# Optimization experiments

Measured on AMD Instinct MI355X. Metric: run time of the kernel, lower is better.

Reference implementation:

```python
import jax, jax.numpy as jnp
import numpy as np

B, T, I, H, L = 128, 512, 512, 1024, 2
KEEP = 0.9  # 1 - dropout_rate


def setup_inputs() -> dict:
    key = jax.random.key(0)
    ks = jax.random.split(key, 13)
    s = 0.02
    bern = lambda k, shape: (jax.random.bernoulli(k, KEEP, shape) / KEEP).astype(jnp.float32)
    return {
        "x": jax.random.normal(ks[0], (B, T, I), dtype=jnp.float32),
        "W_ih0": jax.random.normal(ks[1], (4 * H, I), dtype=jnp.float32) * s,
        "W_hh0": jax.random.normal(ks[2], (4 * H, H), dtype=jnp.float32) * s,
        "b_ih0": jax.random.normal(ks[3], (4 * H,), dtype=jnp.float32) * s,
        "b_hh0": jax.random.normal(ks[4], (4 * H,), dtype=jnp.float32) * s,
        "W_ih1": jax.random.normal(ks[5], (4 * H, H), dtype=jnp.float32) * s,
        "W_hh1": jax.random.normal(ks[6], (4 * H, H), dtype=jnp.float32) * s,
        "b_ih1": jax.random.normal(ks[7], (4 * H,), dtype=jnp.float32) * s,
        "b_hh1": jax.random.normal(ks[8], (4 * H,), dtype=jnp.float32) * s,
        "out_mask": bern(ks[9], (L, B, H)),
        "h_mask": bern(ks[10], (L, B, H)),
        "c_mask": bern(ks[11], (L, B, H)),
    }


def _run_layer(x_tbi, W_ih, W_hh, b_ih, b_hh, om, hm, cm):
    """x_tbi: [T,B,in]; masks: [B,H]. Returns ([T,B,H] outputs, final (h,c))."""
    h0 = jnp.zeros((x_tbi.shape[1], H), dtype=x_tbi.dtype)
    c0 = jnp.zeros_like(h0)
    # precompute input projections for all timesteps: [T,B,4H]
    xg = jnp.einsum('tbi,gi->tbg', x_tbi, W_ih) + b_ih + b_hh

    def step(carry, xg_t):
        h, c = carry
        gates = xg_t + h @ W_hh.T  # [B,4H]
        i, f, g, o = jnp.split(gates, 4, axis=-1)
        i, f, o = jax.nn.sigmoid(i), jax.nn.sigmoid(f), jax.nn.sigmoid(o)
        g = jnp.tanh(g)
        c2 = f * c + i * g
        h2 = o * jnp.tanh(c2)
        out = h2 * om
        return (h2 * hm, c2 * cm), out

    (hf, cf), ys = jax.lax.scan(step, (h0, c0), xg)
    return ys, (hf, cf)


def reference(x, W_ih0, W_hh0, b_ih0, b_hh0, W_ih1, W_hh1, b_ih1, b_hh1,
              out_mask, h_mask, c_mask):
    layers = [(W_ih0, W_hh0, b_ih0, b_hh0), (W_ih1, W_hh1, b_ih1, b_hh1)]
    xt = jnp.transpose(x, (1, 0, 2))  # [T,B,I]
    for l, (Wi, Wh, bi, bh) in enumerate(layers):
        xt, (hf, cf) = _run_layer(xt, Wi, Wh, bi, bh,
                                  out_mask[l], h_mask[l], c_mask[l])
    out = jnp.transpose(xt, (1, 0, 2))  # [B,T,H]
    return out, (hf[None], cf[None])
```

## Files before the change

### kernel.cpp

```cpp
#include <hip/hip_runtime.h>

#define B_  128
#define T_  512
#define I_  512
#define H_  1024
#define G4  4096
#define SLOT 262144L
#define SENTW 0xFFFFFFFFu

typedef __attribute__((ext_vector_type(8))) short   short8;
typedef __attribute__((ext_vector_type(4))) short   short4v;
typedef __attribute__((ext_vector_type(4))) float   f32x4;
typedef unsigned long long u64;

__device__ __forceinline__ float bf2f(short u){
  return __uint_as_float(((unsigned)(unsigned short)u) << 16);
}
__device__ __forceinline__ short f2bf(float f){
  unsigned u = __float_as_uint(f);
  unsigned r = (u + 0x7FFFu + ((u >> 16) & 1u)) >> 16;
  return (short)r;
}
__device__ __forceinline__ float sigm(float x){ return 1.0f/(1.0f + __expf(-x)); }
__device__ __forceinline__ float tanh_(float x){ return 1.0f - 2.0f/(__expf(2.0f*x) + 1.0f); }
__device__ __forceinline__ bool okq(u64 a){
  return ((unsigned)a != SENTW) & ((unsigned)(a >> 32) != SENTW);
}

__global__ __launch_bounds__(256) void cvt_bf16(const float* __restrict__ in,
                                                short* __restrict__ out, int nq){
  int i = blockIdx.x*256 + threadIdx.x;
  if (i >= nq) return;
  float4 v = ((const float4*)in)[i];
  short4v o; o.x = f2bf(v.x); o.y = f2bf(v.y); o.z = f2bf(v.z); o.w = f2bf(v.w);
  ((short4v*)out)[i] = o;
}

__global__ __launch_bounds__(256) void swz_whh(const float* __restrict__ W,
                                               short* __restrict__ out){
  int c = blockIdx.x*256 + threadIdx.x;
  int l = c & 63, ks = (c >> 6) & 15, ct = (c >> 10) & 1, wvv = (c >> 11) & 7, jb = c >> 14;
  int g = wvv >> 1, kh = wvv & 1;
  long row = (long)(g*1024 + jb*32 + ct*16 + (l & 15));
  int col = kh*512 + ks*32 + (l >> 4)*8;
  const float* src = W + row*H_ + col;
  short8 o;
#pragma unroll
  for (int e = 0; e < 8; ++e) o[e] = f2bf(src[e]);
  ((short8*)out)[c] = o;
}

template<int K>
__global__ __launch_bounds__(256) void proj_gemm(const short* __restrict__ A,
                                                 const short* __restrict__ W,
                                                 const float* __restrict__ bih,
                                                 const float* __restrict__ bhh,
                                                 short* __restrict__ C){
  __shared__ __align__(16) short lds[2][2][128*40];
  const int tid = threadIdx.x;
  const int l  = tid & 63, wv = tid >> 6;
  const int wm = wv >> 1,  wn = wv & 1;
  const int nt = blockIdx.x, mt = blockIdx.y;
  const int r0 = tid >> 2, cb = (tid & 3) * 8;
  const short* Ab = A + (long)(mt*128 + r0)*K + cb;
  const short* Wb = W + (long)(nt*128 + r0)*K + cb;
  const int lo  = r0*40 + cb;
  const int lo2 = lo + 64*40;
  const int NK = K/32;

  short8 pa0 = *(const short8*)(Ab);
  short8 pa1 = *(const short8*)(Ab + 64*K);
  short8 pb0 = *(const short8*)(Wb);
  short8 pb1 = *(const short8*)(Wb + 64*K);
  *(short8*)&lds[0][0][lo]  = pa0;
  *(short8*)&lds[0][0][lo2] = pa1;
  *(short8*)&lds[0][1][lo]  = pb0;
  *(short8*)&lds[0][1][lo2] = pb1;

  f32x4 acc[4][4];
  f32x4 z = {0.f,0.f,0.f,0.f};
#pragma unroll
  for (int i = 0; i < 4; ++i)
#pragma unroll
    for (int j = 0; j < 4; ++j) acc[i][j] = z;

  for (int kt = 0; kt < NK; ++kt){
    __syncthreads();
    if (kt + 1 < NK){
      pa0 = *(const short8*)(Ab + (kt+1)*32);
      pa1 = *(const short8*)(Ab + (kt+1)*32 + 64*K);
      pb0 = *(const short8*)(Wb + (kt+1)*32);
      pb1 = *(const short8*)(Wb + (kt+1)*32 + 64*K);
    }
    const short* As = lds[kt & 1][0];
    const short* Bs = lds[kt & 1][1];
    short8 bfr[4];
#pragma unroll
    for (int nf = 0; nf < 4; ++nf)
      bfr[nf] = *(const short8*)&Bs[(wn*64 + nf*16 + (l & 15))*40 + (l >> 4)*8];
#pragma unroll
    for (int mf = 0; mf < 4; ++mf){
      short8 af = *(const short8*)&As[(wm*64 + mf*16 + (l & 15))*40 + (l >> 4)*8];
#pragma unroll
      for (int nf = 0; nf < 4; ++nf)
        acc[mf][nf] = __builtin_amdgcn_mfma_f32_16x16x32_bf16(af, bfr[nf], acc[mf][nf], 0, 0, 0);
    }
    if (kt + 1 < NK){
      int nb = (kt + 1) & 1;
      *(short8*)&lds[nb][0][lo]  = pa0;
      *(short8*)&lds[nb][0][lo2] = pa1;
      *(short8*)&lds[nb][1][lo]  = pb0;
      *(short8*)&lds[nb][1][lo2] = pb1;
    }
  }

  __syncthreads();
  short* cst = (short*)&lds[0][0][0];
#pragma unroll
  for (int nf = 0; nf < 4; ++nf){
    int nc = wn*64 + nf*16 + (l & 15);
    int n  = nt*128 + nc;
    float bs = bih[n] + bhh[n];
#pragma unroll
    for (int mf = 0; mf < 4; ++mf){
#pragma unroll
      for (int r = 0; r < 4; ++r){
        int mr = wm*64 + mf*16 + (l >> 4)*4 + r;
        cst[mr*132 + nc] = f2bf(acc[mf][nf][r] + bs);
      }
    }
  }
  __syncthreads();
  const long m0 = (long)mt*128;
  const int  n0 = nt*128;
#pragma unroll
  for (int i = 0; i < 8; ++i){
    int sid = i*256 + tid;
    int mr = sid >> 4, seg = sid & 15;
    *(short8*)&C[(m0 + mr)*G4 + n0 + seg*8] = *(const short8*)&cst[mr*132 + seg*8];
  }
}

template<int LAYER, bool RING>
__global__ __launch_bounds__(512, 2) void lstm_scan(
    short* __restrict__ hring,
    const short* __restrict__ Wsw, const short* __restrict__ xg,
    const float* __restrict__ om, const float* __restrict__ hm, const float* __restrict__ cm,
    short* __restrict__ out0, float* __restrict__ dout,
    int* __restrict__ flags)
{
  const int tid = threadIdx.x;
  const int l = tid & 63, wv = tid >> 6;
  const int bt = blockIdx.x, jb = blockIdx.y;

  short8 w0[16], w1[16];
  {
    const short8* wp = (const short8*)Wsw + ((long)((jb*8 + wv)*2)*16)*64 + l;
#pragma unroll
    for (int ks = 0; ks < 16; ++ks) w0[ks] = wp[ks*64];
#pragma unroll
    for (int ks = 0; ks < 16; ++ks) w1[ks] = wp[(16 + ks)*64];
    f32x4* wf0 = (f32x4*)w0;
    f32x4* wf1 = (f32x4*)w1;
#pragma unroll
    for (int i = 0; i < 16; ++i){ asm volatile("" : "+v"(wf0[i])); asm volatile("" : "+v"(wf1[i])); }
  }

  const int idx = wv*8 + (l >> 3);
  const int bl  = idx & 15;
  const int jl  = ((idx >> 4) << 3) + (l & 7);
  const int jcol = jb*32 + jl;
  const long bj = (long)(bt*16 + bl)*H_ + jcol;
  const float mo = om[bj], mh = hm[bj], mc = cm[bj];
  float c = 0.f;
  const int ct_r = jl >> 4;
  const int lane_src = (jl & 15) + ((bl >> 2) << 4);
  const int rr = bl & 3;
  const int kh = wv & 1;

  __shared__ __align__(16) short hbuf[2048*8];
  __shared__ float red[16*264];
  __shared__ __align__(16) short sstage[512];
  int* flbase = flags + (long)bt*T_*32;

  const long go0 = (long)(wv*256 + 0*64 + l)*2;
  const long go1 = (long)(wv*256 + 1*64 + l)*2;
  const long go2 = (long)(wv*256 + 2*64 + l)*2;
  const long go3 = (long)(wv*256 + 3*64 + l)*2;

  const long xbase = (long)(bt*16 + bl)*T_*G4 + jcol;
  short xv0 = xg[xbase], xv1 = xg[xbase + H_], xv2 = xg[xbase + 2*H_], xv3 = xg[xbase + 3*H_];

  for (int t = 0; t < T_; ++t){
    const long slotoff  = RING ? (long)t*SLOT     : (long)(t & 1)*SLOT;
    const long nslotoff = RING ? (long)(t+1)*SLOT : (long)((t+1) & 1)*SLOT;

    if (t > 0){
      const u64* hp = (const u64*)((const char*)hring + slotoff + (long)bt*32768);
      if constexpr (RING){
        u64 q0=0,q1=0,q2=0,q3=0,q4=0,q5=0,q6=0,q7=0;
        int ok = 0, spins = 0;
        while (true){
          if (!(ok & 1)){
            u64 a = __hip_atomic_load(hp + go0,     __ATOMIC_RELAXED, __HIP_MEMORY_SCOPE_AGENT);
            u64 b = __hip_atomic_load(hp + go0 + 1, __ATOMIC_RELAXED, __HIP_MEMORY_SCOPE_AGENT);
            if (okq(a) & okq(b)){ q0 = a; q1 = b; ok |= 1; }
          }
          if (!(ok & 2)){
            u64 a = __hip_atomic_load(hp + go1,     __ATOMIC_RELAXED, __HIP_MEMORY_SCOPE_AGENT);
            u64 b = __hip_atomic_load(hp + go1 + 1, __ATOMIC_RELAXED, __HIP_MEMORY_SCOPE_AGENT);
            if (okq(a) & okq(b)){ q2 = a; q3 = b; ok |= 2; }
          }
          if (!(ok & 4)){
            u64 a = __hip_atomic_load(hp + go2,     __ATOMIC_RELAXED, __HIP_MEMORY_SCOPE_AGENT);
            u64 b = __hip_atomic_load(hp + go2 + 1, __ATOMIC_RELAXED, __HIP_MEMORY_SCOPE_AGENT);
            if (okq(a) & okq(b)){ q4 = a; q5 = b; ok |= 4; }
          }
          if (!(ok & 8)){
            u64 a = __hip_atomic_load(hp + go3,     __ATOMIC_RELAXED, __HIP_MEMORY_SCOPE_AGENT);
            u64 b = __hip_atomic_load(hp + go3 + 1, __ATOMIC_RELAXED, __HIP_MEMORY_SCOPE_AGENT);
            if (okq(a) & okq(b)){ q6 = a; q7 = b; ok |= 8; }
          }
          if (ok == 15) break;
          if (++spins > (1 << 20)) break;
          if (spins > 2) __builtin_amdgcn_s_sleep(2);
        }
        union { u64 u[2]; short8 s; } c0, c1, c2_, c3;
        c0.u[0] = q0; c0.u[1] = q1;  c1.u[0] = q2; c1.u[1] = q3;
        c2_.u[0] = q4; c2_.u[1] = q5; c3.u[0] = q6; c3.u[1] = q7;
        *(short8*)&hbuf[(wv*256 +   0 + l)*8] = c0.s;
        *(short8*)&hbuf[(wv*256 +  64 + l)*8] = c1.s;
        *(short8*)&hbuf[(wv*256 + 128 + l)*8] = c2_.s;
        *(short8*)&hbuf[(wv*256 + 192 + l)*8] = c3.s;
      } else {
        short8 vv[4];
#pragma unroll
        for (int i = 0; i < 4; ++i){
          const u64* ap = hp + (long)(wv*256 + i*64 + l)*2;
          union { u64 q[2]; short8 s; } uu;
          uu.q[0] = __hip_atomic_load(ap,     __ATOMIC_RELAXED, __HIP_MEMORY_SCOPE_AGENT);
          uu.q[1] = __hip_atomic_load(ap + 1, __ATOMIC_RELAXED, __HIP_MEMORY_SCOPE_AGENT);
          vv[i] = uu.s;
        }
#pragma unroll
        for (int i = 0; i < 4; ++i)
          *(short8*)&hbuf[(wv*256 + i*64 + l)*8] = vv[i];
      }
      __syncthreads();

      f32x4 a00 = {0.f,0.f,0.f,0.f}, a01 = {0.f,0.f,0.f,0.f};
      f32x4 a10 = {0.f,0.f,0.f,0.f}, a11 = {0.f,0.f,0.f,0.f};
#pragma unroll
      for (int ks = 0; ks < 16; ++ks){
        short8 av = *(const short8*)&hbuf[((kh*16 + ks)*64 + l)*8];
        if (ks & 1){
          a01 = __builtin_amdgcn_mfma_f32_16x16x32_bf16(av, w0[ks], a01, 0, 0, 0);
          a11 = __builtin_amdgcn_mfma_f32_16x16x32_bf16(av, w1[ks], a11, 0, 0, 0);
        } else {
          a00 = __builtin_amdgcn_mfma_f32_16x16x32_bf16(av, w0[ks], a00, 0, 0, 0);
          a10 = __builtin_amdgcn_mfma_f32_16x16x32_bf16(av, w1[ks], a10, 0, 0, 0);
        }
      }
      f32x4 s0, s1;
#pragma unroll
      for (int r = 0; r < 4; ++r){ s0[r] = a00[r] + a01[r]; s1[r] = a10[r] + a11[r]; }
      *(f32x4*)&red[(wv*2 + 0)*264 + l*4] = s0;
      *(f32x4*)&red[(wv*2 + 1)*264 + l*4] = s1;
      __syncthreads();
    }

    float gate[4];
    short xvv[4] = {xv0, xv1, xv2, xv3};
#pragma unroll
    for (int g = 0; g < 4; ++g){
      float rv = 0.f;
      if (t > 0){
        rv = red[((g*2 + 0)*2 + ct_r)*264 + lane_src*4 + rr]
           + red[((g*2 + 1)*2 + ct_r)*264 + lane_src*4 + rr];
      }
      gate[g] = rv + bf2f(xvv[g]);
    }
    float ii = sigm(gate[0]);
    float ff = sigm(gate[1]);
    float gg = tanh_(gate[2]);
    float oo = sigm(gate[3]);
    float c2 = ff*c + ii*gg;
    float h2 = oo*tanh_(c2);
    c = c2*mc;
    float hn = h2*mh;

    if (t == T_ - 1){
      if (LAYER == 0){
        out0[((long)(bt*16 + bl)*T_ + t)*H_ + jcol] = f2bf(h2*mo);
      } else {
        dout[((long)(bt*16 + bl)*T_ + t)*H_ + jcol] = h2*mo;
        dout[(long)B_*T_*H_ + bj] = hn;
        dout[(long)B_*T_*H_ + (long)B_*H_ + bj] = c;
      }
      break;
    }

    sstage[wv*64 + l] = f2bf(hn);
    asm volatile("s_waitcnt lgkmcnt(0)" ::: "memory");
    __builtin_amdgcn_sched_barrier(0);
    if (l < 8){
      short8 pk = *(const short8*)&sstage[wv*64 + l*8];
      char* hdst = (char*)hring + nslotoff
                 + ((long)bt*2048 + jb*64 + wv*8 + l)*16;
      if constexpr (RING){
        asm volatile("global_store_dwordx4 %0, %1, off sc1" :: "v"(hdst), "v"(pk) : "memory");
      } else {
        union { short8 s; u64 q[2]; } uu; uu.s = pk;
        u64* qp = (u64*)hdst;
        __hip_atomic_store(qp,     uu.q[0], __ATOMIC_RELAXED, __HIP_MEMORY_SCOPE_AGENT);
        __hip_atomic_store(qp + 1, uu.q[1], __ATOMIC_RELAXED, __HIP_MEMORY_SCOPE_AGENT);
      }
    }
    if constexpr (!RING){
      asm volatile("s_waitcnt vmcnt(0)" ::: "memory");
      __syncthreads();
      if (tid == 0)
        __hip_atomic_store(&flbase[(long)t*32 + jb], 1,
                           __ATOMIC_RELAXED, __HIP_MEMORY_SCOPE_AGENT);
    }

    if (LAYER == 0){
      out0[((long)(bt*16 + bl)*T_ + t)*H_ + jcol] = f2bf(h2*mo);
    } else {
      dout[((long)(bt*16 + bl)*T_ + t)*H_ + jcol] = h2*mo;
    }
    {
      const short* xp = xg + xbase + (long)(t + 1)*G4;
      xv0 = xp[0]; xv1 = xp[H_]; xv2 = xp[2*H_]; xv3 = xp[3*H_];
    }

    if constexpr (!RING){
      const u64* fp = (const u64*)&flbase[(long)t*32];
      int spins = 0;
      while (true){
        int ok = 1;
        if (l < 16){
          u64 v = __hip_atomic_load(fp + l, __ATOMIC_RELAXED, __HIP_MEMORY_SCOPE_AGENT);
          ok = ((unsigned)v != 0u) & ((unsigned)(v >> 32) != 0u);
        }
        if (__all(ok)) break;
        if (++spins > (1 << 20)) break;
        if (spins > 8) __builtin_amdgcn_s_sleep(1);
      }
      __builtin_amdgcn_sched_barrier(0);
      __builtin_amdgcn_fence(__ATOMIC_ACQUIRE, "workgroup");
    }
  }
}

extern "C" void kernel_launch(void* const* d_in, const int* in_sizes, int n_in,
                              void* d_out, int out_size, void* d_ws, size_t ws_size,
                              hipStream_t stream){
  const float* x    = (const float*)d_in[0];
  const float* Wih0 = (const float*)d_in[1];
  const float* Whh0 = (const float*)d_in[2];
  const float* bih0 = (const float*)d_in[3];
  const float* bhh0 = (const float*)d_in[4];
  const float* Wih1 = (const float*)d_in[5];
  const float* Whh1 = (const float*)d_in[6];
  const float* bih1 = (const float*)d_in[7];
  const float* bhh1 = (const float*)d_in[8];
  const float* omsk = (const float*)d_in[9];
  const float* hmsk = (const float*)d_in[10];
  const float* cmsk = (const float*)d_in[11];
  float* out = (float*)d_out;

  char* p = (char*)d_ws;
  auto alloc = [&](size_t bytes)->char*{
    char* r = p; p += (bytes + 255) & ~(size_t)255; return r;
  };
  short* xg      = (short*)alloc((size_t)65536*4096*2);
  short* out0_bf = (short*)alloc((size_t)67108864*2);
  short* x_bf    = (short*)out0_bf;
  short* wih0_bf = (short*)alloc((size_t)2097152*2);
  short* wih1_bf = (short*)alloc((size_t)4194304*2);
  short* whh0_sw = (short*)alloc((size_t)4194304*2);
  short* whh1_sw = (short*)alloc((size_t)4194304*2);
  int*   flags0  = (int*)alloc((size_t)8*512*32*4);
  int*   flags1  = (int*)alloc((size_t)8*512*32*4);
  size_t fixed = (size_t)(p - (char*)d_ws);
  bool ring = (fixed + (size_t)512*SLOT) <= ws_size;
  size_t ringbytes = ring ? (size_t)512*SLOT : (size_t)2*SLOT;
  short* hring = (short*)alloc(ringbytes);
  if ((size_t)(p - (char*)d_ws) > ws_size) return;

  hipMemsetAsync(flags0, 0, (size_t)8*512*32*4, stream);
  hipMemsetAsync(flags1, 0, (size_t)8*512*32*4, stream);
  hipMemsetAsync(hring, 0xFF, ringbytes, stream);

  cvt_bf16<<<33554432/4/256, 256, 0, stream>>>(x,    x_bf,    33554432/4);
  cvt_bf16<<<2097152/4/256,  256, 0, stream>>>(Wih0, wih0_bf, 2097152/4);
  cvt_bf16<<<4194304/4/256,  256, 0, stream>>>(Wih1, wih1_bf, 4194304/4);
  swz_whh <<<524288/256,     256, 0, stream>>>(Whh0, whh0_sw);
  swz_whh <<<524288/256,     256, 0, stream>>>(Whh1, whh1_sw);

  proj_gemm<512><<<dim3(32, 512), 256, 0, stream>>>(x_bf, wih0_bf, bih0, bhh0, xg);
  if (ring)
    lstm_scan<0, true ><<<dim3(8, 32), 512, 0, stream>>>(hring, whh0_sw, xg,
        omsk, hmsk, cmsk, out0_bf, nullptr, flags0);
  else
    lstm_scan<0, false><<<dim3(8, 32), 512, 0, stream>>>(hring, whh0_sw, xg,
        omsk, hmsk, cmsk, out0_bf, nullptr, flags0);

  hipMemsetAsync(hring, 0xFF, ringbytes, stream);

  proj_gemm<1024><<<dim3(32, 512), 256, 0, stream>>>(out0_bf, wih1_bf, bih1, bhh1, xg);
  if (ring)
    lstm_scan<1, true ><<<dim3(8, 32), 512, 0, stream>>>(hring, whh1_sw, xg,
        omsk + 131072, hmsk + 131072, cmsk + 131072, nullptr, out, flags1);
  else
    lstm_scan<1, false><<<dim3(8, 32), 512, 0, stream>>>(hring, whh1_sw, xg,
        omsk + 131072, hmsk + 131072, cmsk + 131072, nullptr, out, flags1);
}
```

Before: 4.101 ms.

## Replace sentinel polling on LSTM ring data with per-wave ready marks

The ring path of the LSTM scan used to poll the hidden-state data itself until no 0xFF sentinel words remained. Now each wave writes a ready mark after storing its slice, and one wave per block polls the 256 marks before a barrier and plain loads of the hidden state. This removes the two large 0xFF memsets of the ring buffer and the per-element sentinel checks. In exchange it adds a block barrier and a second memory round trip per step, and correctness depends on the partial vmcnt wait ordering the h store before the mark store.

```diff
diff --git a/kernel.cpp b/kernel.cpp
--- a/kernel.cpp
+++ b/kernel.cpp
@@ -6,7 +6,6 @@
 #define H_  1024
 #define G4  4096
 #define SLOT 262144L
-#define SENTW 0xFFFFFFFFu
 
 typedef __attribute__((ext_vector_type(8))) short   short8;
 typedef __attribute__((ext_vector_type(4))) short   short4v;
@@ -23,9 +22,6 @@
 }
 __device__ __forceinline__ float sigm(float x){ return 1.0f/(1.0f + __expf(-x)); }
 __device__ __forceinline__ float tanh_(float x){ return 1.0f - 2.0f/(__expf(2.0f*x) + 1.0f); }
-__device__ __forceinline__ bool okq(u64 a){
-  return ((unsigned)a != SENTW) & ((unsigned)(a >> 32) != SENTW);
-}
 
 __global__ __launch_bounds__(256) void cvt_bf16(const float* __restrict__ in,
                                                 short* __restrict__ out, int nq){
@@ -147,6 +143,7 @@
     const short* __restrict__ Wsw, const short* __restrict__ xg,
     const float* __restrict__ om, const float* __restrict__ hm, const float* __restrict__ cm,
     short* __restrict__ out0, float* __restrict__ dout,
+    int* __restrict__ marks,
     int* __restrict__ flags)
 {
   const int tid = threadIdx.x;
@@ -183,11 +180,6 @@
   __shared__ __align__(16) short sstage[512];
   int* flbase = flags + (long)bt*T_*32;
 
-  const long go0 = (long)(wv*256 + 0*64 + l)*2;
-  const long go1 = (long)(wv*256 + 1*64 + l)*2;
-  const long go2 = (long)(wv*256 + 2*64 + l)*2;
-  const long go3 = (long)(wv*256 + 3*64 + l)*2;
-
   const long xbase = (long)(bt*16 + bl)*T_*G4 + jcol;
   short xv0 = xg[xbase], xv1 = xg[xbase + H_], xv2 = xg[xbase + 2*H_], xv3 = xg[xbase + 3*H_];
 
@@ -196,43 +188,31 @@
     const long nslotoff = RING ? (long)(t+1)*SLOT : (long)((t+1) & 1)*SLOT;
 
     if (t > 0){
-      const u64* hp = (const u64*)((const char*)hring + slotoff + (long)bt*32768);
       if constexpr (RING){
-        u64 q0=0,q1=0,q2=0,q3=0,q4=0,q5=0,q6=0,q7=0;
-        int ok = 0, spins = 0;
-        while (true){
-          if (!(ok & 1)){
-            u64 a = __hip_atomic_load(hp + go0,     __ATOMIC_RELAXED, __HIP_MEMORY_SCOPE_AGENT);
-            u64 b = __hip_atomic_load(hp + go0 + 1, __ATOMIC_RELAXED, __HIP_MEMORY_SCOPE_AGENT);
-            if (okq(a) & okq(b)){ q0 = a; q1 = b; ok |= 1; }
+        if (wv == 0){
+          const u64* mk = (const u64*)(marks + ((long)bt*T_ + (t - 1))*256);
+          int spins = 0;
+          while (true){
+            u64 a = __hip_atomic_load(mk + l,      __ATOMIC_RELAXED, __HIP_MEMORY_SCOPE_AGENT);
+            u64 b = __hip_atomic_load(mk + 64 + l, __ATOMIC_RELAXED, __HIP_MEMORY_SCOPE_AGENT);
+            unsigned m = (unsigned)a & (unsigned)(a >> 32) & (unsigned)b & (unsigned)(b >> 32);
+            if (__all(m != 0)) break;
+            if (++spins > (1 << 20)) break;
+            if (spins > 8) __builtin_amdgcn_s_sleep(1);
           }
-          if (!(ok & 2)){
-            u64 a = __hip_atomic_load(hp + go1,     __ATOMIC_RELAXED, __HIP_MEMORY_SCOPE_AGENT);
-            u64 b = __hip_atomic_load(hp + go1 + 1, __ATOMIC_RELAXED, __HIP_MEMORY_SCOPE_AGENT);
-            if (okq(a) & okq(b)){ q2 = a; q3 = b; ok |= 2; }
-          }
-          if (!(ok & 4)){
-            u64 a = __hip_atomic_load(hp + go2,     __ATOMIC_RELAXED, __HIP_MEMORY_SCOPE_AGENT);
-            u64 b = __hip_atomic_load(hp + go2 + 1, __ATOMIC_RELAXED, __HIP_MEMORY_SCOPE_AGENT);
-            if (okq(a) & okq(b)){ q4 = a; q5 = b; ok |= 4; }
-          }
-          if (!(ok & 8)){
-            u64 a = __hip_atomic_load(hp + go3,     __ATOMIC_RELAXED, __HIP_MEMORY_SCOPE_AGENT);
-            u64 b = __hip_atomic_load(hp + go3 + 1, __ATOMIC_RELAXED, __HIP_MEMORY_SCOPE_AGENT);
-            if (okq(a) & okq(b)){ q6 = a; q7 = b; ok |= 8; }
-          }
-          if (ok == 15) break;
-          if (++spins > (1 << 20)) break;
-          if (spins > 2) __builtin_amdgcn_s_sleep(2);
         }
-        union { u64 u[2]; short8 s; } c0, c1, c2_, c3;
-        c0.u[0] = q0; c0.u[1] = q1;  c1.u[0] = q2; c1.u[1] = q3;
-        c2_.u[0] = q4; c2_.u[1] = q5; c3.u[0] = q6; c3.u[1] = q7;
-        *(short8*)&hbuf[(wv*256 +   0 + l)*8] = c0.s;
-        *(short8*)&hbuf[(wv*256 +  64 + l)*8] = c1.s;
-        *(short8*)&hbuf[(wv*256 + 128 + l)*8] = c2_.s;
-        *(short8*)&hbuf[(wv*256 + 192 + l)*8] = c3.s;
+        __syncthreads();
+        __builtin_amdgcn_fence(__ATOMIC_ACQUIRE, "workgroup");
+        const char* hsl = (const char*)hring + slotoff + (long)bt*32768;
+        short8 vv[4];
+#pragma unroll
+        for (int i = 0; i < 4; ++i)
+          vv[i] = *(const short8*)(hsl + (long)(wv*256 + i*64 + l)*16);
+#pragma unroll
+        for (int i = 0; i < 4; ++i)
+          *(short8*)&hbuf[(wv*256 + i*64 + l)*8] = vv[i];
       } else {
+        const u64* hp = (const u64*)((const char*)hring + slotoff + (long)bt*32768);
         short8 vv[4];
 #pragma unroll
         for (int i = 0; i < 4; ++i){
@@ -316,25 +296,38 @@
         __hip_atomic_store(qp + 1, uu.q[1], __ATOMIC_RELAXED, __HIP_MEMORY_SCOPE_AGENT);
       }
     }
-    if constexpr (!RING){
+
+    if constexpr (RING){
+      if (LAYER == 0){
+        out0[((long)(bt*16 + bl)*T_ + t)*H_ + jcol] = f2bf(h2*mo);
+      } else {
+        dout[((long)(bt*16 + bl)*T_ + t)*H_ + jcol] = h2*mo;
+      }
+      {
+        const short* xp = xg + xbase + (long)(t + 1)*G4;
+        xv0 = xp[0]; xv1 = xp[H_]; xv2 = xp[2*H_]; xv3 = xp[3*H_];
+      }
+      asm volatile("s_waitcnt vmcnt(5)" ::: "memory");
+      if (l == 0){
+        int one = 1;
+        int* mp = marks + ((long)bt*T_ + t)*256 + jb*8 + wv;
+        asm volatile("global_store_dword %0, %1, off sc1" :: "v"(mp), "v"(one) : "memory");
+      }
+    } else {
       asm volatile("s_waitcnt vmcnt(0)" ::: "memory");
       __syncthreads();
       if (tid == 0)
         __hip_atomic_store(&flbase[(long)t*32 + jb], 1,
                            __ATOMIC_RELAXED, __HIP_MEMORY_SCOPE_AGENT);
-    }
-
-    if (LAYER == 0){
-      out0[((long)(bt*16 + bl)*T_ + t)*H_ + jcol] = f2bf(h2*mo);
-    } else {
-      dout[((long)(bt*16 + bl)*T_ + t)*H_ + jcol] = h2*mo;
-    }
-    {
-      const short* xp = xg + xbase + (long)(t + 1)*G4;
-      xv0 = xp[0]; xv1 = xp[H_]; xv2 = xp[2*H_]; xv3 = xp[3*H_];
-    }
-
-    if constexpr (!RING){
+      if (LAYER == 0){
+        out0[((long)(bt*16 + bl)*T_ + t)*H_ + jcol] = f2bf(h2*mo);
+      } else {
+        dout[((long)(bt*16 + bl)*T_ + t)*H_ + jcol] = h2*mo;
+      }
+      {
+        const short* xp = xg + xbase + (long)(t + 1)*G4;
+        xv0 = xp[0]; xv1 = xp[H_]; xv2 = xp[2*H_]; xv3 = xp[3*H_];
+      }
       const u64* fp = (const u64*)&flbase[(long)t*32];
       int spins = 0;
       while (true){
@@ -381,6 +374,8 @@
   short* wih1_bf = (short*)alloc((size_t)4194304*2);
   short* whh0_sw = (short*)alloc((size_t)4194304*2);
   short* whh1_sw = (short*)alloc((size_t)4194304*2);
+  int*   marks0  = (int*)alloc((size_t)8*512*256*4);
+  int*   marks1  = (int*)alloc((size_t)8*512*256*4);
   int*   flags0  = (int*)alloc((size_t)8*512*32*4);
   int*   flags1  = (int*)alloc((size_t)8*512*32*4);
   size_t fixed = (size_t)(p - (char*)d_ws);
@@ -389,9 +384,10 @@
   short* hring = (short*)alloc(ringbytes);
   if ((size_t)(p - (char*)d_ws) > ws_size) return;
 
+  hipMemsetAsync(marks0, 0, (size_t)8*512*256*4, stream);
+  hipMemsetAsync(marks1, 0, (size_t)8*512*256*4, stream);
   hipMemsetAsync(flags0, 0, (size_t)8*512*32*4, stream);
   hipMemsetAsync(flags1, 0, (size_t)8*512*32*4, stream);
-  hipMemsetAsync(hring, 0xFF, ringbytes, stream);
 
   cvt_bf16<<<33554432/4/256, 256, 0, stream>>>(x,    x_bf,    33554432/4);
   cvt_bf16<<<2097152/4/256,  256, 0, stream>>>(Wih0, wih0_bf, 2097152/4);
@@ -402,18 +398,16 @@
   proj_gemm<512><<<dim3(32, 512), 256, 0, stream>>>(x_bf, wih0_bf, bih0, bhh0, xg);
   if (ring)
     lstm_scan<0, true ><<<dim3(8, 32), 512, 0, stream>>>(hring, whh0_sw, xg,
-        omsk, hmsk, cmsk, out0_bf, nullptr, flags0);
+        omsk, hmsk, cmsk, out0_bf, nullptr, marks0, flags0);
   else
     lstm_scan<0, false><<<dim3(8, 32), 512, 0, stream>>>(hring, whh0_sw, xg,
-        omsk, hmsk, cmsk, out0_bf, nullptr, flags0);
-
-  hipMemsetAsync(hring, 0xFF, ringbytes, stream);
+        omsk, hmsk, cmsk, out0_bf, nullptr, marks0, flags0);
 
   proj_gemm<1024><<<dim3(32, 512), 256, 0, stream>>>(out0_bf, wih1_bf, bih1, bhh1, xg);
   if (ring)
     lstm_scan<1, true ><<<dim3(8, 32), 512, 0, stream>>>(hring, whh1_sw, xg,
-        omsk + 131072, hmsk + 131072, cmsk + 131072, nullptr, out, flags1);
+        omsk + 131072, hmsk + 131072, cmsk + 131072, nullptr, out, marks1, flags1);
   else
     lstm_scan<1, false><<<dim3(8, 32), 512, 0, stream>>>(hring, whh1_sw, xg,
-        omsk + 131072, hmsk + 131072, cmsk + 131072, nullptr, out, flags1);
-}
+        omsk + 131072, hmsk + 131072, cmsk + 131072, nullptr, out, marks1, flags1);
+}
```

Result: slower. 7.079 ms (+72.6%).
